# Kernel optimization log

Measured on AMD Instinct MI355X. Metric: run time of the kernel, lower is better.

## Reference

```python
import jax, jax.numpy as jnp
import numpy as np

B, T, N, C, H = 64, 12, 1370, 8, 64

def setup_inputs() -> dict:
    key = jax.random.key(0)
    ks = jax.random.split(key, 7)
    s_ih = 1.0 / np.sqrt(H)
    inp = {
        "x": jax.random.normal(ks[0], (B, T, N, C), dtype=jnp.float32),
        # PyTorch nn.LSTM params, gate order (i, f, g, o)
        "W_ih": jax.random.uniform(ks[1], (4 * H, C), jnp.float32, -s_ih, s_ih),
        "W_hh": jax.random.uniform(ks[2], (4 * H, H), jnp.float32, -s_ih, s_ih),
        "b_ih": jax.random.uniform(ks[3], (4 * H,), jnp.float32, -s_ih, s_ih),
        "b_hh": jax.random.uniform(ks[4], (4 * H,), jnp.float32, -s_ih, s_ih),
        "W_fc": jax.random.uniform(ks[5], (C, H), jnp.float32, -s_ih, s_ih),
        "b_fc": jax.random.uniform(ks[6], (C,), jnp.float32, -s_ih, s_ih),
    }
    return inp

def reference(x, W_ih, W_hh, b_ih, b_hh, W_fc, b_fc):
    Bx, Tx, Nx, Cx = x.shape
    Hh = W_hh.shape[1]
    # (B, T, N, C) -> (B*N, T, C): shared-weight LSTM over all node sequences
    xr = jnp.transpose(x, (0, 2, 1, 3)).reshape(Bx * Nx, Tx, Cx)
    # Precompute input projections for all timesteps: (B*N, T, 4H)
    x_gates = jnp.einsum('btc,gc->btg', xr, W_ih) + b_ih
    # time-major for scan: (T, B*N, 4H)
    x_gates = jnp.moveaxis(x_gates, 1, 0)

    def step(carry, xg):
        h, c = carry
        gates = xg + h @ W_hh.T + b_hh  # (B*N, 4H)
        i, f, g, o = jnp.split(gates, 4, axis=-1)
        i = jax.nn.sigmoid(i)
        f = jax.nn.sigmoid(f)
        g = jnp.tanh(g)
        o = jax.nn.sigmoid(o)
        c = f * c + i * g
        h = o * jnp.tanh(c)
        return (h, c), None

    h0 = jnp.zeros((Bx * Nx, Hh), dtype=x.dtype)
    c0 = jnp.zeros((Bx * Nx, Hh), dtype=x.dtype)
    (h_last, _), _ = jax.lax.scan(step, (h0, c0), x_gates)

    y_flat = h_last @ W_fc.T + b_fc  # (B*N, C)
    return y_flat.reshape(Bx, Nx, Cx)
```

## Files before the change

kernel.cpp:

```cpp
#include <hip/hip_runtime.h>

#define T_ 12
#define N_ 1370
#define MSEQ 32
#define LDA 88
#define HBUF (MSEQ * LDA)
#define NBLK 2740

typedef __attribute__((ext_vector_type(8))) short short8;
typedef __attribute__((ext_vector_type(4))) float floatx4;

#define NLOG2E -1.4426950408889634f
#define TLOG2E 2.8853900817779268f

__device__ __forceinline__ short f2bf(float x) {
  unsigned u = __builtin_bit_cast(unsigned, x);
  u = (u + 0x7fffu + ((u >> 16) & 1u)) >> 16;
  return (short)u;
}
__device__ __forceinline__ unsigned pk_bf16(float a, float b) {
  unsigned r;
  asm("v_cvt_pk_bf16_f32 %0, %1, %2" : "=v"(r) : "v"(a), "v"(b));
  return r;
}
__device__ __forceinline__ short8 load_w8s(const float* __restrict__ p, float s) {
  short8 r;
#pragma unroll
  for (int j = 0; j < 8; ++j) r[j] = f2bf(p[j] * s);
  return r;
}

__global__ void __launch_bounds__(256, 4) lstm_kernel(
    const float* __restrict__ x, const float* __restrict__ W_ih,
    const float* __restrict__ W_hh, const float* __restrict__ b_ih,
    const float* __restrict__ b_hh, const float* __restrict__ W_fc,
    const float* __restrict__ b_fc, float* __restrict__ out) {
  __shared__ short hbuf[2 * HBUF + 8];

  const int tid = threadIdx.x;
  const int wave = tid >> 6;
  const int lane = tid & 63;
  const int m16 = lane & 15;
  const int q = lane >> 4;
  const int blk = blockIdx.x;

  const int xseq = tid >> 3, xc = tid & 7;
  unsigned xpk[6];
  {
    const int s0 = blk * MSEQ + xseq;
    const int bidx = s0 / N_;
    const int nidx = s0 - bidx * N_;
    const float* xp = x + ((size_t)(bidx * T_) * N_ + nidx) * 8 + xc;
    float xv[T_];
#pragma unroll
    for (int t = 0; t < T_; ++t) xv[t] = xp[(size_t)t * (N_ * 8)];
#pragma unroll
    for (int i = 0; i < 6; ++i) xpk[i] = pk_bf16(xv[2 * i], xv[2 * i + 1]);
  }

  const int urow = wave * 16 + m16;
  short8 wA[4][3];
#pragma unroll
  for (int g = 0; g < 4; ++g) {
    const float sg = (g == 2) ? TLOG2E : NLOG2E;
    const int grow = g * 64 + urow;
    const float* wr = W_hh + grow * 64;
    wA[g][0] = load_w8s(wr + q * 8, sg);
    wA[g][1] = load_w8s(wr + 32 + q * 8, sg);
    short8 z = {0, 0, 0, 0, 0, 0, 0, 0};
    if (q == 0) {
      wA[g][2] = load_w8s(W_ih + grow * 8, sg);
    } else if (q == 1) {
      z[0] = f2bf(sg * (b_ih[grow] + b_hh[grow]));
      wA[g][2] = z;
    } else {
      wA[g][2] = z;
    }
  }

  {
    int* hp = (int*)hbuf;
#pragma unroll
    for (int i = tid; i < (2 * HBUF + 8) / 2; i += 256) hp[i] = 0;
  }
  __syncthreads();
  if (tid < 2 * MSEQ)
    hbuf[(tid >> 5) * HBUF + (tid & 31) * LDA + 72] = (short)0x3F80;
  hbuf[xseq * LDA + 64 + xc] = (short)xpk[0];
  __syncthreads();

  const floatx4 zacc = {0.0f, 0.0f, 0.0f, 0.0f};
  float cst[2][4];
#pragma unroll
  for (int nt = 0; nt < 2; ++nt)
#pragma unroll
    for (int r = 0; r < 4; ++r) cst[nt][r] = 0.0f;

#pragma unroll
  for (int t = 0; t < T_; ++t) {
    const int rb = t & 1, wb = rb ^ 1;
    if (t + 1 < T_) {
      unsigned p = xpk[(t + 1) >> 1];
      short xv = (short)(((t + 1) & 1) ? (p >> 16) : p);
      hbuf[wb * HBUF + xseq * LDA + 64 + xc] = xv;
    }
#pragma unroll
    for (int nt = 0; nt < 2; ++nt) {
      const int srow = nt * 16 + m16;
      const short* base = &hbuf[rb * HBUF + srow * LDA];
      short8 b0 = *(const short8*)(base + q * 8);
      short8 b1 = *(const short8*)(base + 32 + q * 8);
      short8 b2 = *(const short8*)(base + 64 + q * 8);
      floatx4 gi = __builtin_amdgcn_mfma_f32_16x16x32_bf16(wA[0][0], b0, zacc, 0, 0, 0);
      floatx4 gf = __builtin_amdgcn_mfma_f32_16x16x32_bf16(wA[1][0], b0, zacc, 0, 0, 0);
      floatx4 gg = __builtin_amdgcn_mfma_f32_16x16x32_bf16(wA[2][0], b0, zacc, 0, 0, 0);
      floatx4 go = __builtin_amdgcn_mfma_f32_16x16x32_bf16(wA[3][0], b0, zacc, 0, 0, 0);
      gi = __builtin_amdgcn_mfma_f32_16x16x32_bf16(wA[0][1], b1, gi, 0, 0, 0);
      gf = __builtin_amdgcn_mfma_f32_16x16x32_bf16(wA[1][1], b1, gf, 0, 0, 0);
      gg = __builtin_amdgcn_mfma_f32_16x16x32_bf16(wA[2][1], b1, gg, 0, 0, 0);
      go = __builtin_amdgcn_mfma_f32_16x16x32_bf16(wA[3][1], b1, go, 0, 0, 0);
      gi = __builtin_amdgcn_mfma_f32_16x16x32_bf16(wA[0][2], b2, gi, 0, 0, 0);
      gf = __builtin_amdgcn_mfma_f32_16x16x32_bf16(wA[1][2], b2, gf, 0, 0, 0);
      gg = __builtin_amdgcn_mfma_f32_16x16x32_bf16(wA[2][2], b2, gg, 0, 0, 0);
      go = __builtin_amdgcn_mfma_f32_16x16x32_bf16(wA[3][2], b2, go, 0, 0, 0);
      float hv[4];
#pragma unroll
      for (int r = 0; r < 4; ++r) {
        float di = 1.0f + __builtin_amdgcn_exp2f(gi[r]);
        float df = 1.0f + __builtin_amdgcn_exp2f(gf[r]);
        float dg = 1.0f + __builtin_amdgcn_exp2f(gg[r]);
        float dq = 1.0f + __builtin_amdgcn_exp2f(go[r]);
        float pa = di * df, pb = dg * dq;
        float rp = __builtin_amdgcn_rcpf(pa * pb);
        float iv = rp * df * pb;
        float fv = rp * di * pb;
        float t1 = rp * pa;
        float gv = fmaf(-2.0f, t1 * dq, 1.0f);
        float ov = t1 * dg;
        float cc = fmaf(fv, cst[nt][r], iv * gv);
        cst[nt][r] = cc;
        float dt = 1.0f + __builtin_amdgcn_exp2f(cc * TLOG2E);
        float tc = fmaf(-2.0f, __builtin_amdgcn_rcpf(dt), 1.0f);
        hv[r] = ov * tc;
      }
      unsigned long long pk =
          (unsigned long long)pk_bf16(hv[0], hv[1]) |
          ((unsigned long long)pk_bf16(hv[2], hv[3]) << 32);
      *(unsigned long long*)&hbuf[wb * HBUF + srow * LDA + wave * 16 + q * 4] = pk;
    }
    __syncthreads();
  }

  if (wave < 2) {
    short8 f0, f1;
    short8 z = {0, 0, 0, 0, 0, 0, 0, 0};
    if (m16 < 8) {
      const float* wr = W_fc + m16 * 64;
      f0 = load_w8s(wr + q * 8, 1.0f);
      f1 = load_w8s(wr + 32 + q * 8, 1.0f);
    } else {
      f0 = z;
      f1 = z;
    }
    const int srow = wave * 16 + m16;
    short8 h0 = *(const short8*)&hbuf[srow * LDA + q * 8];
    short8 h1 = *(const short8*)&hbuf[srow * LDA + 32 + q * 8];
    floatx4 acc = __builtin_amdgcn_mfma_f32_16x16x32_bf16(f0, h0, zacc, 0, 0, 0);
    acc = __builtin_amdgcn_mfma_f32_16x16x32_bf16(f1, h1, acc, 0, 0, 0);
    if (q < 2) {
      const int orow = blk * MSEQ + srow;
#pragma unroll
      for (int r = 0; r < 4; ++r)
        out[orow * 8 + q * 4 + r] = acc[r] + b_fc[q * 4 + r];
    }
  }
}

extern "C" void kernel_launch(void* const* d_in, const int* in_sizes, int n_in,
                              void* d_out, int out_size, void* d_ws,
                              size_t ws_size, hipStream_t stream) {
  const float* x    = (const float*)d_in[0];
  const float* W_ih = (const float*)d_in[1];
  const float* W_hh = (const float*)d_in[2];
  const float* b_ih = (const float*)d_in[3];
  const float* b_hh = (const float*)d_in[4];
  const float* W_fc = (const float*)d_in[5];
  const float* b_fc = (const float*)d_in[6];
  float* out = (float*)d_out;
  hipLaunchKernelGGL(lstm_kernel, dim3(NBLK), dim3(256), 0, stream,
                     x, W_ih, W_hh, b_ih, b_hh, W_fc, b_fc, out);
}
```

Before: 173.1 us.

## Process two 32-sequence groups per block to amortize weight setup and barriers

Each block now handles 64 sequences split into two independent 32-row groups, with separate double-buffered LDS regions, and the four MFMA tiles are interleaved per timestep. This halves the grid, so per-block setup (weight conversion into registers, LDS init) and the per-step __syncthreads are amortized over twice the work. The interleaving gives the scheduler independent MFMA/transcendental chains to hide latency. In exchange it doubles LDS and cell-state registers per block, which may reduce occupancy, and leaves fewer blocks to spread across CUs.

```diff
diff --git a/kernel.cpp b/kernel.cpp
--- a/kernel.cpp
+++ b/kernel.cpp
@@ -2,10 +2,8 @@
 
 #define T_ 12
 #define N_ 1370
-#define MSEQ 32
 #define LDA 88
-#define HBUF (MSEQ * LDA)
-#define NBLK 2740
+#define NBLK 1370
 
 typedef __attribute__((ext_vector_type(8))) short short8;
 typedef __attribute__((ext_vector_type(4))) float floatx4;
@@ -35,7 +33,7 @@
     const float* __restrict__ W_hh, const float* __restrict__ b_ih,
     const float* __restrict__ b_hh, const float* __restrict__ W_fc,
     const float* __restrict__ b_fc, float* __restrict__ out) {
-  __shared__ short hbuf[2 * HBUF + 8];
+  __shared__ short hbuf[2 * 2 * 32 * LDA + 8];
 
   const int tid = threadIdx.x;
   const int wave = tid >> 6;
@@ -44,18 +42,24 @@
   const int q = lane >> 4;
   const int blk = blockIdx.x;
 
+#define HROW(G, B, R) (&hbuf[(((G)*2 + (B)) * 32 + (R)) * LDA])
+
   const int xseq = tid >> 3, xc = tid & 7;
-  unsigned xpk[6];
+  unsigned xpkA[6], xpkB[6];
   {
-    const int s0 = blk * MSEQ + xseq;
-    const int bidx = s0 / N_;
-    const int nidx = s0 - bidx * N_;
-    const float* xp = x + ((size_t)(bidx * T_) * N_ + nidx) * 8 + xc;
-    float xv[T_];
-#pragma unroll
-    for (int t = 0; t < T_; ++t) xv[t] = xp[(size_t)t * (N_ * 8)];
-#pragma unroll
-    for (int i = 0; i < 6; ++i) xpk[i] = pk_bf16(xv[2 * i], xv[2 * i + 1]);
+#pragma unroll
+    for (int g2 = 0; g2 < 2; ++g2) {
+      const int s0 = blk * 64 + g2 * 32 + xseq;
+      const int bidx = s0 / N_;
+      const int nidx = s0 - bidx * N_;
+      const float* xp = x + ((size_t)(bidx * T_) * N_ + nidx) * 8 + xc;
+      float xv[T_];
+#pragma unroll
+      for (int t = 0; t < T_; ++t) xv[t] = xp[(size_t)t * (N_ * 8)];
+      unsigned* dst = g2 ? xpkB : xpkA;
+#pragma unroll
+      for (int i = 0; i < 6; ++i) dst[i] = pk_bf16(xv[2 * i], xv[2 * i + 1]);
+    }
   }
 
   const int urow = wave * 16 + m16;
@@ -81,77 +85,86 @@
   {
     int* hp = (int*)hbuf;
 #pragma unroll
-    for (int i = tid; i < (2 * HBUF + 8) / 2; i += 256) hp[i] = 0;
+    for (int i = tid; i < (2 * 2 * 32 * LDA + 8) / 2; i += 256) hp[i] = 0;
   }
   __syncthreads();
-  if (tid < 2 * MSEQ)
-    hbuf[(tid >> 5) * HBUF + (tid & 31) * LDA + 72] = (short)0x3F80;
-  hbuf[xseq * LDA + 64 + xc] = (short)xpk[0];
+  if (tid < 128)
+    HROW(tid >> 6, (tid >> 5) & 1, tid & 31)[72] = (short)0x3F80;
+  HROW(0, 0, xseq)[64 + xc] = (short)xpkA[0];
+  HROW(1, 0, xseq)[64 + xc] = (short)xpkB[0];
   __syncthreads();
 
   const floatx4 zacc = {0.0f, 0.0f, 0.0f, 0.0f};
-  float cst[2][4];
-#pragma unroll
-  for (int nt = 0; nt < 2; ++nt)
-#pragma unroll
-    for (int r = 0; r < 4; ++r) cst[nt][r] = 0.0f;
+  float cst[2][2][4];
+#pragma unroll
+  for (int g2 = 0; g2 < 2; ++g2)
+#pragma unroll
+    for (int nt = 0; nt < 2; ++nt)
+#pragma unroll
+      for (int r = 0; r < 4; ++r) cst[g2][nt][r] = 0.0f;
+
+#define TILE(G, NT, rb, wb)                                                    \
+  do {                                                                         \
+    const int srow = (NT)*16 + m16;                                            \
+    const short* base = HROW((G), (rb), srow);                                 \
+    short8 b0 = *(const short8*)(base + q * 8);                                \
+    short8 b1 = *(const short8*)(base + 32 + q * 8);                           \
+    short8 b2 = *(const short8*)(base + 64 + q * 8);                           \
+    floatx4 gi = __builtin_amdgcn_mfma_f32_16x16x32_bf16(wA[0][0], b0, zacc, 0, 0, 0); \
+    floatx4 gf = __builtin_amdgcn_mfma_f32_16x16x32_bf16(wA[1][0], b0, zacc, 0, 0, 0); \
+    floatx4 gg = __builtin_amdgcn_mfma_f32_16x16x32_bf16(wA[2][0], b0, zacc, 0, 0, 0); \
+    floatx4 go = __builtin_amdgcn_mfma_f32_16x16x32_bf16(wA[3][0], b0, zacc, 0, 0, 0); \
+    gi = __builtin_amdgcn_mfma_f32_16x16x32_bf16(wA[0][1], b1, gi, 0, 0, 0);   \
+    gf = __builtin_amdgcn_mfma_f32_16x16x32_bf16(wA[1][1], b1, gf, 0, 0, 0);   \
+    gg = __builtin_amdgcn_mfma_f32_16x16x32_bf16(wA[2][1], b1, gg, 0, 0, 0);   \
+    go = __builtin_amdgcn_mfma_f32_16x16x32_bf16(wA[3][1], b1, go, 0, 0, 0);   \
+    gi = __builtin_amdgcn_mfma_f32_16x16x32_bf16(wA[0][2], b2, gi, 0, 0, 0);   \
+    gf = __builtin_amdgcn_mfma_f32_16x16x32_bf16(wA[1][2], b2, gf, 0, 0, 0);   \
+    gg = __builtin_amdgcn_mfma_f32_16x16x32_bf16(wA[2][2], b2, gg, 0, 0, 0);   \
+    go = __builtin_amdgcn_mfma_f32_16x16x32_bf16(wA[3][2], b2, go, 0, 0, 0);   \
+    float hv[4];                                                               \
+    _Pragma("unroll") for (int r = 0; r < 4; ++r) {                            \
+      float di = 1.0f + __builtin_amdgcn_exp2f(gi[r]);                         \
+      float df = 1.0f + __builtin_amdgcn_exp2f(gf[r]);                         \
+      float dg = 1.0f + __builtin_amdgcn_exp2f(gg[r]);                         \
+      float dq = 1.0f + __builtin_amdgcn_exp2f(go[r]);                         \
+      float pa = di * df, pb = dg * dq;                                        \
+      float rp = __builtin_amdgcn_rcpf(pa * pb);                               \
+      float iv = rp * df * pb;                                                 \
+      float fv = rp * di * pb;                                                 \
+      float t1 = rp * pa;                                                      \
+      float gv = fmaf(-2.0f, t1 * dq, 1.0f);                                   \
+      float ov = t1 * dg;                                                      \
+      float cc = fmaf(fv, cst[G][NT][r], iv * gv);                             \
+      cst[G][NT][r] = cc;                                                      \
+      float dt = 1.0f + __builtin_amdgcn_exp2f(cc * TLOG2E);                   \
+      float tc = fmaf(-2.0f, __builtin_amdgcn_rcpf(dt), 1.0f);                 \
+      hv[r] = ov * tc;                                                         \
+    }                                                                          \
+    unsigned long long pk =                                                    \
+        (unsigned long long)pk_bf16(hv[0], hv[1]) |                            \
+        ((unsigned long long)pk_bf16(hv[2], hv[3]) << 32);                     \
+    *(unsigned long long*)(HROW((G), (wb), srow) + wave * 16 + q * 4) = pk;    \
+  } while (0)
 
 #pragma unroll
   for (int t = 0; t < T_; ++t) {
     const int rb = t & 1, wb = rb ^ 1;
     if (t + 1 < T_) {
-      unsigned p = xpk[(t + 1) >> 1];
-      short xv = (short)(((t + 1) & 1) ? (p >> 16) : p);
-      hbuf[wb * HBUF + xseq * LDA + 64 + xc] = xv;
-    }
-#pragma unroll
-    for (int nt = 0; nt < 2; ++nt) {
-      const int srow = nt * 16 + m16;
-      const short* base = &hbuf[rb * HBUF + srow * LDA];
-      short8 b0 = *(const short8*)(base + q * 8);
-      short8 b1 = *(const short8*)(base + 32 + q * 8);
-      short8 b2 = *(const short8*)(base + 64 + q * 8);
-      floatx4 gi = __builtin_amdgcn_mfma_f32_16x16x32_bf16(wA[0][0], b0, zacc, 0, 0, 0);
-      floatx4 gf = __builtin_amdgcn_mfma_f32_16x16x32_bf16(wA[1][0], b0, zacc, 0, 0, 0);
-      floatx4 gg = __builtin_amdgcn_mfma_f32_16x16x32_bf16(wA[2][0], b0, zacc, 0, 0, 0);
-      floatx4 go = __builtin_amdgcn_mfma_f32_16x16x32_bf16(wA[3][0], b0, zacc, 0, 0, 0);
-      gi = __builtin_amdgcn_mfma_f32_16x16x32_bf16(wA[0][1], b1, gi, 0, 0, 0);
-      gf = __builtin_amdgcn_mfma_f32_16x16x32_bf16(wA[1][1], b1, gf, 0, 0, 0);
-      gg = __builtin_amdgcn_mfma_f32_16x16x32_bf16(wA[2][1], b1, gg, 0, 0, 0);
-      go = __builtin_amdgcn_mfma_f32_16x16x32_bf16(wA[3][1], b1, go, 0, 0, 0);
-      gi = __builtin_amdgcn_mfma_f32_16x16x32_bf16(wA[0][2], b2, gi, 0, 0, 0);
-      gf = __builtin_amdgcn_mfma_f32_16x16x32_bf16(wA[1][2], b2, gf, 0, 0, 0);
-      gg = __builtin_amdgcn_mfma_f32_16x16x32_bf16(wA[2][2], b2, gg, 0, 0, 0);
-      go = __builtin_amdgcn_mfma_f32_16x16x32_bf16(wA[3][2], b2, go, 0, 0, 0);
-      float hv[4];
-#pragma unroll
-      for (int r = 0; r < 4; ++r) {
-        float di = 1.0f + __builtin_amdgcn_exp2f(gi[r]);
-        float df = 1.0f + __builtin_amdgcn_exp2f(gf[r]);
-        float dg = 1.0f + __builtin_amdgcn_exp2f(gg[r]);
-        float dq = 1.0f + __builtin_amdgcn_exp2f(go[r]);
-        float pa = di * df, pb = dg * dq;
-        float rp = __builtin_amdgcn_rcpf(pa * pb);
-        float iv = rp * df * pb;
-        float fv = rp * di * pb;
-        float t1 = rp * pa;
-        float gv = fmaf(-2.0f, t1 * dq, 1.0f);
-        float ov = t1 * dg;
-        float cc = fmaf(fv, cst[nt][r], iv * gv);
-        cst[nt][r] = cc;
-        float dt = 1.0f + __builtin_amdgcn_exp2f(cc * TLOG2E);
-        float tc = fmaf(-2.0f, __builtin_amdgcn_rcpf(dt), 1.0f);
-        hv[r] = ov * tc;
-      }
-      unsigned long long pk =
-          (unsigned long long)pk_bf16(hv[0], hv[1]) |
-          ((unsigned long long)pk_bf16(hv[2], hv[3]) << 32);
-      *(unsigned long long*)&hbuf[wb * HBUF + srow * LDA + wave * 16 + q * 4] = pk;
-    }
+      unsigned pA = xpkA[(t + 1) >> 1], pB = xpkB[(t + 1) >> 1];
+      short vA = (short)(((t + 1) & 1) ? (pA >> 16) : pA);
+      short vB = (short)(((t + 1) & 1) ? (pB >> 16) : pB);
+      HROW(0, wb, xseq)[64 + xc] = vA;
+      HROW(1, wb, xseq)[64 + xc] = vB;
+    }
+    TILE(0, 0, rb, wb);
+    TILE(1, 0, rb, wb);
+    TILE(0, 1, rb, wb);
+    TILE(1, 1, rb, wb);
     __syncthreads();
   }
 
-  if (wave < 2) {
+  {
     short8 f0, f1;
     short8 z = {0, 0, 0, 0, 0, 0, 0, 0};
     if (m16 < 8) {
@@ -162,13 +175,15 @@
       f0 = z;
       f1 = z;
     }
-    const int srow = wave * 16 + m16;
-    short8 h0 = *(const short8*)&hbuf[srow * LDA + q * 8];
-    short8 h1 = *(const short8*)&hbuf[srow * LDA + 32 + q * 8];
+    const int grp = wave >> 1, mt = wave & 1;
+    const int srow = mt * 16 + m16;
+    const short* ar = HROW(grp, 0, srow);
+    short8 h0 = *(const short8*)(ar + q * 8);
+    short8 h1 = *(const short8*)(ar + 32 + q * 8);
     floatx4 acc = __builtin_amdgcn_mfma_f32_16x16x32_bf16(f0, h0, zacc, 0, 0, 0);
     acc = __builtin_amdgcn_mfma_f32_16x16x32_bf16(f1, h1, acc, 0, 0, 0);
     if (q < 2) {
-      const int orow = blk * MSEQ + srow;
+      const int orow = blk * 64 + grp * 32 + srow;
 #pragma unroll
       for (int r = 0; r < 4; ++r)
         out[orow * 8 + q * 4 + r] = acc[r] + b_fc[q * 4 + r];
```

Measured after the change: 179.9 us. +3.9%, slower.
